# Kernel optimization log

Measured on AMD Instinct MI355X. Metric: run time of the kernel, lower is better.

The kernel has to match this reference:

```python
import jax, jax.numpy as jnp
import numpy as np
import math

B, L, E, H, G = 2, 128, 1024, 16, 8
D = E // H   # head_dim = 64
R = H // G   # query heads per kv head = 2


def setup_inputs() -> dict:
    key = jax.random.key(0)
    ks = jax.random.split(key, 12)
    def nrm(k, shape, s=1.0):
        return jax.random.normal(k, shape, dtype=jnp.float32) * s
    return {
        "Q": nrm(ks[0], (B, L, E)),
        "K": nrm(ks[1], (B, L, E)),
        "V": nrm(ks[2], (B, L, E)),
        "rpe": nrm(ks[3], (B, L, L, E)),
        "ln_g": jnp.ones((E,), jnp.float32),
        "ln_b": jnp.zeros((E,), jnp.float32),
        "Wq": nrm(ks[4], (E, H * D), 0.02), "bq": jnp.zeros((H * D,), jnp.float32),
        "Wk": nrm(ks[5], (E, G * D), 0.02), "bk": jnp.zeros((G * D,), jnp.float32),
        "Wv": nrm(ks[6], (E, G * D), 0.02), "bv": jnp.zeros((G * D,), jnp.float32),
        "Wrk": nrm(ks[7], (E, G * D), 0.02), "brk": jnp.zeros((G * D,), jnp.float32),
        "Wrv": nrm(ks[8], (E, G * D), 0.02), "brv": jnp.zeros((G * D,), jnp.float32),
        "Wo": nrm(ks[9], (E, E), 0.02), "bo": jnp.zeros((E,), jnp.float32),
    }


def _layernorm(x, g, b, eps=1e-5):
    mu = jnp.mean(x, axis=-1, keepdims=True)
    var = jnp.var(x, axis=-1, keepdims=True)
    return (x - mu) * jax.lax.rsqrt(var + eps) * g + b


def reference(Q, K, V, rpe, ln_g, ln_b, Wq, bq, Wk, bk, Wv, bv, Wrk, brk, Wrv, brv, Wo, bo):
    q = (Q @ Wq + bq).reshape(B, L, H, D).transpose(0, 2, 1, 3)   # [B,H,L,D]
    k = (K @ Wk + bk).reshape(B, L, G, D).transpose(0, 2, 1, 3)   # [B,G,L,D]
    v = (V @ Wv + bv).reshape(B, L, G, D).transpose(0, 2, 1, 3)   # [B,G,L,D]

    rn = _layernorm(rpe, ln_g, ln_b)                              # [B,L,L,E]
    rpe_k = (rn @ Wrk + brk).reshape(B, L, L, G, D).transpose(0, 3, 1, 2, 4)  # [B,G,L,L,D]
    rpe_v = (rn @ Wrv + brv).reshape(B, L, L, G, D).transpose(0, 3, 1, 2, 4)

    # Group query heads: head h = g*R + r maps to kv group g (repeat_interleave semantics).
    qg = q.reshape(B, G, R, L, D)
    # score[b,h,i,j] = q[b,h,i] . (k[b,g,i] + rpe_k[b,g,i,j]) / sqrt(D)
    # (note: the original pairs q_i with k_i, only rpe_k carries j-dependence)
    base = jnp.einsum('bgrid,bgid->bgri', qg, k)                  # j-independent q.k
    cross = jnp.einsum('bgrid,bgijd->bgrij', qg, rpe_k)
    scores = (base[..., None] + cross) / math.sqrt(D)             # [B,G,R,L,L]

    # Faithful to F.softmax over flattened L*L axis per head.
    attn = jax.nn.softmax(scores.reshape(B, G, R, L * L), axis=-1).reshape(B, G, R, L, L)

    # qv[b,h,i] = sum_j attn[b,h,i,j] * (v[b,g,i] + rpe_v[b,g,i,j])
    wsum = jnp.sum(attn, axis=-1)                                 # [B,G,R,L]
    qv = wsum[..., None] * v[:, :, None] + jnp.einsum('bgrij,bgijd->bgrid', attn, rpe_v)
    qv = qv.reshape(B, H, L, D).transpose(0, 2, 1, 3).reshape(B, L, E)
    return qv @ Wo + bo
```

## Files before the change

kernel.cpp:

```cpp
#include <hip/hip_runtime.h>


__global__ __launch_bounds__(256) void k_zero(
    const float* __restrict__ bq, const float* __restrict__ bk, const float* __restrict__ bv,
    const float* __restrict__ bo,
    float* __restrict__ q_ws, float* __restrict__ k_ws, float* __restrict__ v_ws,
    float* __restrict__ qv_ws, float* __restrict__ out, float* __restrict__ Gu_ws)
{
  int rr = blockIdx.x, tid = threadIdx.x;
#pragma unroll
  for (int s = 0; s < 4; s++) {
    int i = tid + s * 256;
    q_ws[rr * 1024 + i] = bq[i];
    qv_ws[rr * 1024 + i] = 0.f;
    out[rr * 1024 + i] = bo[i];
  }
#pragma unroll
  for (int s = 0; s < 2; s++) {
    int i = tid + s * 256;
    k_ws[rr * 512 + i] = bk[i];
    v_ws[rr * 512 + i] = bv[i];
  }
  int t = rr * 256 + tid;
  if (t < 4096) Gu_ws[t] = 0.f;
}

__global__ __launch_bounds__(256) void k_qkv(
    const float* __restrict__ Q, const float* __restrict__ K, const float* __restrict__ V,
    const float* __restrict__ Wq, const float* __restrict__ Wk, const float* __restrict__ Wv,
    float* __restrict__ q_ws, float* __restrict__ k_ws, float* __restrict__ v_ws)
{
  __shared__ float xs[8][256];
  int ct = blockIdx.x, rt = blockIdx.y, es = blockIdx.z, tid = threadIdx.x;
  const float* X; const float* W; float* out; int ldW, ldO, c0;
  if (ct < 4)      { X = Q; W = Wq; out = q_ws; ldW = 1024; ldO = 1024; c0 = ct * 256; }
  else if (ct < 6) { X = K; W = Wk; out = k_ws; ldW = 512;  ldO = 512;  c0 = (ct - 4) * 256; }
  else             { X = V; W = Wv; out = v_ws; ldW = 512;  ldO = 512;  c0 = (ct - 6) * 256; }
  int row0 = rt * 8, e0 = es * 256;
  for (int f = tid; f < 512; f += 256) {
    int r = f >> 6, e4 = f & 63;
    *(float4*)&xs[r][e4 * 4] = *(const float4*)(X + (size_t)(row0 + r) * 1024 + e0 + e4 * 4);
  }
  __syncthreads();
  int cg = tid & 63, rs = tid >> 6;
  int c = c0 + cg * 4;
  float a0[4] = {0, 0, 0, 0}, a1[4] = {0, 0, 0, 0};
  for (int e = 0; e < 256; e++) {
    float4 w4 = *(const float4*)(W + (size_t)(e0 + e) * ldW + c);
    float x0 = xs[rs][e], x1 = xs[rs + 4][e];
    a0[0] += x0 * w4.x; a0[1] += x0 * w4.y; a0[2] += x0 * w4.z; a0[3] += x0 * w4.w;
    a1[0] += x1 * w4.x; a1[1] += x1 * w4.y; a1[2] += x1 * w4.z; a1[3] += x1 * w4.w;
  }
#pragma unroll
  for (int s = 0; s < 4; s++) {
    atomicAdd(out + (size_t)(row0 + rs) * ldO + c + s, a0[s]);
    atomicAdd(out + (size_t)(row0 + rs + 4) * ldO + c + s, a1[s]);
  }
}

__global__ __launch_bounds__(256) void k_base(
    const float* __restrict__ q_ws, const float* __restrict__ k_ws,
    const float* __restrict__ brk, float* __restrict__ S0_ws)
{
  int t = blockIdx.x * 256 + threadIdx.x;
  int r = t >> 4, h = t & 15, g = h >> 1;
  const float* qp = q_ws + r * 1024 + h * 64;
  const float* kp = k_ws + r * 512 + g * 64;
  const float* bp = brk + g * 64;
  float s = 0.f;
  for (int d = 0; d < 64; d++) s += qp[d] * (kp[d] + bp[d]);
  S0_ws[t] = s * 0.125f;
}

__global__ __launch_bounds__(256) void k_uproj(
    const float* __restrict__ q_ws, const float* __restrict__ Wrk,
    const float* __restrict__ lng, const float* __restrict__ lnb,
    float* __restrict__ ut_ws, float* __restrict__ Gu_ws, float* __restrict__ S0_ws)
{
  __shared__ float wt[64][132];
  __shared__ float qs[64][65];
  int et = blockIdx.x, rrt = blockIdx.y, g = blockIdx.z, tid = threadIdx.x;
  int e0 = et * 128, rr0 = rrt * 32;
  for (int f = tid; f < 2048; f += 256) {
    int er = f >> 4, dq = f & 15;
    float4 p = *(const float4*)(Wrk + (size_t)(e0 + er) * 512 + g * 64 + dq * 4);
    wt[dq * 4 + 0][er] = p.x; wt[dq * 4 + 1][er] = p.y;
    wt[dq * 4 + 2][er] = p.z; wt[dq * 4 + 3][er] = p.w;
  }
  for (int f = tid; f < 1024; f += 256) {
    int m = f >> 4, dq = f & 15;
    int rr = rr0 + (m >> 1), h = g * 2 + (m & 1);
    float4 p = *(const float4*)(q_ws + (size_t)rr * 1024 + h * 64 + dq * 4);
    qs[m][dq * 4 + 0] = p.x; qs[m][dq * 4 + 1] = p.y;
    qs[m][dq * 4 + 2] = p.z; qs[m][dq * 4 + 3] = p.w;
  }
  __syncthreads();
  int eg = tid & 31, rs = tid >> 5;
  float acc[8][4];
#pragma unroll
  for (int i = 0; i < 8; i++)
#pragma unroll
    for (int s = 0; s < 4; s++) acc[i][s] = 0.f;
  for (int d = 0; d < 64; d++) {
    float4 wv = *(float4*)&wt[d][eg * 4];
#pragma unroll
    for (int i = 0; i < 8; i++) {
      float qv = qs[rs * 8 + i][d];
      acc[i][0] += qv * wv.x; acc[i][1] += qv * wv.y;
      acc[i][2] += qv * wv.z; acc[i][3] += qv * wv.w;
    }
  }
#pragma unroll
  for (int i = 0; i < 4; i++) {
    int m0 = rs * 8 + 2 * i;
    int rr = rr0 + (m0 >> 1);
#pragma unroll
    for (int s = 0; s < 4; s++) {
      int e = e0 + eg * 4 + s;
      float2 st;
      st.x = acc[2 * i][s] * 0.125f;
      st.y = acc[2 * i + 1][s] * 0.125f;
      *(float2*)(ut_ws + ((size_t)rr * 1024 + e) * 16 + g * 2) = st;
    }
  }
  float4 ge4 = *(const float4*)(lng + e0 + eg * 4);
  float4 be4 = *(const float4*)(lnb + e0 + eg * 4);
#pragma unroll
  for (int i = 0; i < 8; i++) {
    float pg = 0.125f * (ge4.x * acc[i][0] + ge4.y * acc[i][1] + ge4.z * acc[i][2] + ge4.w * acc[i][3]);
    float pb = 0.125f * (be4.x * acc[i][0] + be4.y * acc[i][1] + be4.z * acc[i][2] + be4.w * acc[i][3]);
#pragma unroll
    for (int mk = 16; mk >= 1; mk >>= 1) { pg += __shfl_xor(pg, mk); pb += __shfl_xor(pb, mk); }
    if (eg == 0) {
      int m = rs * 8 + i;
      int rr = rr0 + (m >> 1), h = g * 2 + (m & 1);
      atomicAdd(Gu_ws + rr * 16 + h, pg);
      atomicAdd(S0_ws + rr * 16 + h, pb);
    }
  }
}

__global__ __launch_bounds__(128) void k_dotp(
    const float* __restrict__ rpe, const float* __restrict__ lng,
    const float* __restrict__ ut_ws, const float* __restrict__ Gu_ws,
    const float* __restrict__ S0_ws,
    float* __restrict__ s_ws, float* __restrict__ mu_ws, float* __restrict__ rs_ws)
{
  __shared__ float xs[32][140];
  __shared__ float us[128][16];
  int jt = blockIdx.x, rr = blockIdx.y, tid = threadIdx.x;
  int es2 = tid & 1, hg = (tid >> 1) & 3, jp = tid >> 3;
  int j0 = jp * 2;
  float acc0[4] = {0, 0, 0, 0}, acc1[4] = {0, 0, 0, 0};
  float sx0 = 0.f, sq0 = 0.f, sx1 = 0.f, sq1 = 0.f;

  for (int ec = 0; ec < 8; ec++) {
    __syncthreads();
    for (int f = tid; f < 512; f += 128) {
      int e = f >> 2, hq = f & 3;
      float4 u4 = *(const float4*)(ut_ws + ((size_t)rr * 1024 + ec * 128 + e) * 16 + hq * 4);
      float ge = lng[ec * 128 + e];
      u4.x *= ge; u4.y *= ge; u4.z *= ge; u4.w *= ge;
      *(float4*)&us[e][hq * 4] = u4;
    }
    for (int f = tid; f < 1024; f += 128) {
      int j = f >> 5, e4 = f & 31;
      int slot = (e4 < 16) ? e4 * 4 : e4 * 4 + 4;
      *(float4*)&xs[j][slot] =
          *(const float4*)(rpe + ((size_t)(rr * 128 + jt * 32 + j)) * 1024 + ec * 128 + e4 * 4);
    }
    __syncthreads();
    int ebase = es2 * 68, ubase = es2 * 64;
    for (int e4 = 0; e4 < 16; e4++) {
      float4 xa = *(float4*)&xs[j0][ebase + e4 * 4];
      float4 xb = *(float4*)&xs[j0 + 1][ebase + e4 * 4];
      float4 u0 = *(float4*)&us[ubase + e4 * 4 + 0][hg * 4];
      float4 u1 = *(float4*)&us[ubase + e4 * 4 + 1][hg * 4];
      float4 u2 = *(float4*)&us[ubase + e4 * 4 + 2][hg * 4];
      float4 u3 = *(float4*)&us[ubase + e4 * 4 + 3][hg * 4];
      acc0[0] += xa.x * u0.x + xa.y * u1.x + xa.z * u2.x + xa.w * u3.x;
      acc0[1] += xa.x * u0.y + xa.y * u1.y + xa.z * u2.y + xa.w * u3.y;
      acc0[2] += xa.x * u0.z + xa.y * u1.z + xa.z * u2.z + xa.w * u3.z;
      acc0[3] += xa.x * u0.w + xa.y * u1.w + xa.z * u2.w + xa.w * u3.w;
      acc1[0] += xb.x * u0.x + xb.y * u1.x + xb.z * u2.x + xb.w * u3.x;
      acc1[1] += xb.x * u0.y + xb.y * u1.y + xb.z * u2.y + xb.w * u3.y;
      acc1[2] += xb.x * u0.z + xb.y * u1.z + xb.z * u2.z + xb.w * u3.z;
      acc1[3] += xb.x * u0.w + xb.y * u1.w + xb.z * u2.w + xb.w * u3.w;
      sx0 += xa.x + xa.y + xa.z + xa.w;
      sq0 += xa.x * xa.x + xa.y * xa.y + xa.z * xa.z + xa.w * xa.w;
      sx1 += xb.x + xb.y + xb.z + xb.w;
      sq1 += xb.x * xb.x + xb.y * xb.y + xb.z * xb.z + xb.w * xb.w;
    }
  }
#pragma unroll
  for (int s = 0; s < 4; s++) {
    acc0[s] += __shfl_xor(acc0[s], 1);
    acc1[s] += __shfl_xor(acc1[s], 1);
  }
  sx0 += __shfl_xor(sx0, 1); sq0 += __shfl_xor(sq0, 1);
  sx1 += __shfl_xor(sx1, 1); sq1 += __shfl_xor(sq1, 1);

  float4 Gu4 = *(const float4*)(Gu_ws + rr * 16 + hg * 4);
  float4 S04 = *(const float4*)(S0_ws + rr * 16 + hg * 4);
  float mu0 = sx0 * (1.f / 1024.f), mu1 = sx1 * (1.f / 1024.f);
  float r0 = rsqrtf(fmaxf(sq0 * (1.f / 1024.f) - mu0 * mu0, 0.f) + 1e-5f);
  float r1 = rsqrtf(fmaxf(sq1 * (1.f / 1024.f) - mu1 * mu1, 0.f) + 1e-5f);
  int jg0 = jt * 32 + j0;
  if (es2 == 0) {
    float4 o0, o1;
    o0.x = S04.x + r0 * (acc0[0] - mu0 * Gu4.x); o0.y = S04.y + r0 * (acc0[1] - mu0 * Gu4.y);
    o0.z = S04.z + r0 * (acc0[2] - mu0 * Gu4.z); o0.w = S04.w + r0 * (acc0[3] - mu0 * Gu4.w);
    o1.x = S04.x + r1 * (acc1[0] - mu1 * Gu4.x); o1.y = S04.y + r1 * (acc1[1] - mu1 * Gu4.y);
    o1.z = S04.z + r1 * (acc1[2] - mu1 * Gu4.z); o1.w = S04.w + r1 * (acc1[3] - mu1 * Gu4.w);
    *(float4*)(s_ws + ((size_t)rr * 128 + jg0) * 16 + hg * 4) = o0;
    *(float4*)(s_ws + ((size_t)rr * 128 + jg0 + 1) * 16 + hg * 4) = o1;
    if (hg == 0) {
      mu_ws[rr * 128 + jg0] = mu0; rs_ws[rr * 128 + jg0] = r0;
      mu_ws[rr * 128 + jg0 + 1] = mu1; rs_ws[rr * 128 + jg0 + 1] = r1;
    }
  }
}

__global__ __launch_bounds__(256) void k_attn_p(
    const float* __restrict__ mu_ws, const float* __restrict__ rs_ws,
    float* __restrict__ s_ws,
    float* __restrict__ M_ws, float* __restrict__ Z_ws, float* __restrict__ C1_ws)
{
  int rr = blockIdx.x, tid = threadIdx.x;
  int h = tid >> 4, jl = tid & 15;
  float sv[8];
  float m = -1e30f;
#pragma unroll
  for (int k = 0; k < 8; k++) {
    int j = jl + k * 16;
    sv[k] = s_ws[((size_t)rr * 128 + j) * 16 + h];
    m = fmaxf(m, sv[k]);
  }
#pragma unroll
  for (int mk = 8; mk >= 1; mk >>= 1) m = fmaxf(m, __shfl_xor(m, mk, 16));
  float z = 0.f, c1 = 0.f;
#pragma unroll
  for (int k = 0; k < 8; k++) {
    int j = jl + k * 16;
    float p = expf(sv[k] - m);
    z += p;
    float p2 = p * rs_ws[rr * 128 + j];
    c1 += p2 * mu_ws[rr * 128 + j];
    s_ws[((size_t)rr * 128 + j) * 16 + h] = p2;
  }
#pragma unroll
  for (int mk = 8; mk >= 1; mk >>= 1) { z += __shfl_xor(z, mk, 16); c1 += __shfl_xor(c1, mk, 16); }
  if (jl == 0) {
    M_ws[rr * 16 + h] = m; Z_ws[rr * 16 + h] = z; C1_ws[rr * 16 + h] = c1;
  }
}

__global__ __launch_bounds__(256) void k_comb(
    const float* __restrict__ M_ws, const float* __restrict__ Z_ws, float* __restrict__ sc_ws)
{
  __shared__ float Mg[32], Zg[32];
  int tid = threadIdx.x;
  if (tid < 32) {
    int b = tid >> 4, h = tid & 15;
    float m = -1e30f;
    for (int i = 0; i < 128; i++) m = fmaxf(m, M_ws[((b << 7) + i) * 16 + h]);
    float z = 0.f;
    for (int i = 0; i < 128; i++) {
      int idx = ((b << 7) + i) * 16 + h;
      z += Z_ws[idx] * expf(M_ws[idx] - m);
    }
    Mg[tid] = m; Zg[tid] = z;
  }
  __syncthreads();
  for (int idx = tid; idx < 4096; idx += 256) {
    int r = idx >> 4, h = idx & 15, b = r >> 7;
    sc_ws[idx] = expf(M_ws[idx] - Mg[b * 16 + h]) / Zg[b * 16 + h];
  }
}

__global__ __launch_bounds__(256) void k_wun(
    const float* __restrict__ rpe, const float* __restrict__ lng, const float* __restrict__ lnb,
    const float* __restrict__ p2_ws,
    const float* __restrict__ Z_ws, const float* __restrict__ C1_ws,
    float* __restrict__ w_ws)
{
  __shared__ float xs[8][520];
  __shared__ float p2s[128][16];
  __shared__ float C1S[16], ZS[16];
  int et = blockIdx.x, rr = blockIdx.y, tid = threadIdx.x;
  int e0 = et * 512;
  for (int f = tid; f < 512; f += 256) {
    int j = f >> 2, hq = f & 3;
    *(float4*)&p2s[j][hq * 4] = *(const float4*)(p2_ws + ((size_t)rr * 128 + j) * 16 + hq * 4);
  }
  if (tid < 16) { C1S[tid] = C1_ws[rr * 16 + tid]; ZS[tid] = Z_ws[rr * 16 + tid]; }
  float acc[2][16];
#pragma unroll
  for (int c = 0; c < 2; c++)
#pragma unroll
    for (int h = 0; h < 16; h++) acc[c][h] = 0.f;
  for (int jc = 0; jc < 16; jc++) {
    __syncthreads();
    for (int f = tid; f < 1024; f += 256) {
      int j = f >> 7, e4 = f & 127;
      *(float4*)&xs[j][e4 * 4] =
          *(const float4*)(rpe + ((size_t)(rr * 128 + jc * 8 + j)) * 1024 + e0 + e4 * 4);
    }
    __syncthreads();
#pragma unroll
    for (int j = 0; j < 8; j++) {
      float2 x2 = *(float2*)&xs[j][tid * 2];
      float4 p0 = *(float4*)&p2s[jc * 8 + j][0];
      float4 p1 = *(float4*)&p2s[jc * 8 + j][4];
      float4 p2 = *(float4*)&p2s[jc * 8 + j][8];
      float4 p3 = *(float4*)&p2s[jc * 8 + j][12];
      acc[0][0] += x2.x * p0.x; acc[0][1] += x2.x * p0.y; acc[0][2] += x2.x * p0.z; acc[0][3] += x2.x * p0.w;
      acc[0][4] += x2.x * p1.x; acc[0][5] += x2.x * p1.y; acc[0][6] += x2.x * p1.z; acc[0][7] += x2.x * p1.w;
      acc[0][8] += x2.x * p2.x; acc[0][9] += x2.x * p2.y; acc[0][10] += x2.x * p2.z; acc[0][11] += x2.x * p2.w;
      acc[0][12] += x2.x * p3.x; acc[0][13] += x2.x * p3.y; acc[0][14] += x2.x * p3.z; acc[0][15] += x2.x * p3.w;
      acc[1][0] += x2.y * p0.x; acc[1][1] += x2.y * p0.y; acc[1][2] += x2.y * p0.z; acc[1][3] += x2.y * p0.w;
      acc[1][4] += x2.y * p1.x; acc[1][5] += x2.y * p1.y; acc[1][6] += x2.y * p1.z; acc[1][7] += x2.y * p1.w;
      acc[1][8] += x2.y * p2.x; acc[1][9] += x2.y * p2.y; acc[1][10] += x2.y * p2.z; acc[1][11] += x2.y * p2.w;
      acc[1][12] += x2.y * p3.x; acc[1][13] += x2.y * p3.y; acc[1][14] += x2.y * p3.z; acc[1][15] += x2.y * p3.w;
    }
  }
  int e = e0 + tid * 2;
#pragma unroll
  for (int c = 0; c < 2; c++) {
    float ge = lng[e + c], be = lnb[e + c];
    float* wp = w_ws + ((size_t)rr * 1024 + e + c) * 16;
#pragma unroll
    for (int hq = 0; hq < 4; hq++) {
      float4 o;
      o.x = ge * (acc[c][hq * 4 + 0] - C1S[hq * 4 + 0]) + be * ZS[hq * 4 + 0];
      o.y = ge * (acc[c][hq * 4 + 1] - C1S[hq * 4 + 1]) + be * ZS[hq * 4 + 1];
      o.z = ge * (acc[c][hq * 4 + 2] - C1S[hq * 4 + 2]) + be * ZS[hq * 4 + 2];
      o.w = ge * (acc[c][hq * 4 + 3] - C1S[hq * 4 + 3]) + be * ZS[hq * 4 + 3];
      *(float4*)(wp + hq * 4) = o;
    }
  }
}

__global__ __launch_bounds__(256) void k_qv(
    const float* __restrict__ w_ws, const float* __restrict__ Wrv,
    float* __restrict__ qv_ws)
{
  __shared__ float wch[2][256][16];
  int ec = blockIdx.x, rp = blockIdx.y, tid = threadIdx.x;
  int e0 = ec * 256, rr0 = rp * 2;
  for (int f = tid; f < 2048; f += 256) {
    int r2 = f >> 10, rem = f & 1023;
    int e = rem >> 2, hq = rem & 3;
    *(float4*)&wch[r2][e][hq * 4] =
        *(const float4*)(w_ws + ((size_t)(rr0 + r2) * 1024 + e0 + e) * 16 + hq * 4);
  }
  __syncthreads();
  int cg = tid & 127, es2 = tid >> 7;
  int c = cg * 4, g = cg >> 4, h0 = g * 2, dloc = (cg & 15) * 4;
  float a[2][2][4];
#pragma unroll
  for (int r = 0; r < 2; r++)
#pragma unroll
    for (int hh = 0; hh < 2; hh++)
#pragma unroll
      for (int s = 0; s < 4; s++) a[r][hh][s] = 0.f;
  for (int ei = 0; ei < 128; ei++) {
    int e = es2 * 128 + ei;
    float4 wv = *(const float4*)(Wrv + (size_t)(e0 + e) * 512 + c);
    float2 w0 = *(float2*)&wch[0][e][h0];
    float2 w1 = *(float2*)&wch[1][e][h0];
    a[0][0][0] += w0.x * wv.x; a[0][0][1] += w0.x * wv.y; a[0][0][2] += w0.x * wv.z; a[0][0][3] += w0.x * wv.w;
    a[0][1][0] += w0.y * wv.x; a[0][1][1] += w0.y * wv.y; a[0][1][2] += w0.y * wv.z; a[0][1][3] += w0.y * wv.w;
    a[1][0][0] += w1.x * wv.x; a[1][0][1] += w1.x * wv.y; a[1][0][2] += w1.x * wv.z; a[1][0][3] += w1.x * wv.w;
    a[1][1][0] += w1.y * wv.x; a[1][1][1] += w1.y * wv.y; a[1][1][2] += w1.y * wv.z; a[1][1][3] += w1.y * wv.w;
  }
#pragma unroll
  for (int r = 0; r < 2; r++)
#pragma unroll
    for (int hh = 0; hh < 2; hh++)
#pragma unroll
      for (int s = 0; s < 4; s++)
        atomicAdd(qv_ws + (size_t)(rr0 + r) * 1024 + (h0 + hh) * 64 + dloc + s, a[r][hh][s]);
}

__global__ __launch_bounds__(256) void k_out(
    const float* __restrict__ qv_ws, const float* __restrict__ v_ws,
    const float* __restrict__ brv, const float* __restrict__ Z_ws,
    const float* __restrict__ sc_ws, const float* __restrict__ Wo,
    float* __restrict__ out)
{
  __shared__ float xs[8][256];
  int ct = blockIdx.x, rt = blockIdx.y, es = blockIdx.z, tid = threadIdx.x;
  int row0 = rt * 8, e0 = es * 256, c0 = ct * 256;
  for (int f = tid; f < 2048; f += 256) {
    int r = f >> 8, ei = f & 255;
    int e = e0 + ei, row = row0 + r;
    int h = e >> 6, gg = h >> 1, dl = e & 63;
    float vb = v_ws[row * 512 + gg * 64 + dl] + brv[gg * 64 + dl];
    xs[r][ei] = sc_ws[row * 16 + h] * (Z_ws[row * 16 + h] * vb + qv_ws[(size_t)row * 1024 + e]);
  }
  __syncthreads();
  int cg = tid & 63, rs = tid >> 6;
  int c = c0 + cg * 4;
  float a0[4] = {0, 0, 0, 0}, a1[4] = {0, 0, 0, 0};
  for (int e = 0; e < 256; e++) {
    float4 w4 = *(const float4*)(Wo + (size_t)(e0 + e) * 1024 + c);
    float x0 = xs[rs][e], x1 = xs[rs + 4][e];
    a0[0] += x0 * w4.x; a0[1] += x0 * w4.y; a0[2] += x0 * w4.z; a0[3] += x0 * w4.w;
    a1[0] += x1 * w4.x; a1[1] += x1 * w4.y; a1[2] += x1 * w4.z; a1[3] += x1 * w4.w;
  }
#pragma unroll
  for (int s = 0; s < 4; s++) {
    atomicAdd(out + (size_t)(row0 + rs) * 1024 + c + s, a0[s]);
    atomicAdd(out + (size_t)(row0 + rs + 4) * 1024 + c + s, a1[s]);
  }
}

extern "C" void kernel_launch(void* const* d_in, const int* in_sizes, int n_in,
                              void* d_out, int out_size, void* d_ws, size_t ws_size,
                              hipStream_t stream) {
  (void)in_sizes; (void)n_in; (void)out_size; (void)ws_size;
  const float* Q   = (const float*)d_in[0];
  const float* K   = (const float*)d_in[1];
  const float* V   = (const float*)d_in[2];
  const float* rpe = (const float*)d_in[3];
  const float* lng = (const float*)d_in[4];
  const float* lnb = (const float*)d_in[5];
  const float* Wq  = (const float*)d_in[6];
  const float* bq  = (const float*)d_in[7];
  const float* Wk  = (const float*)d_in[8];
  const float* bk  = (const float*)d_in[9];
  const float* Wv  = (const float*)d_in[10];
  const float* bv  = (const float*)d_in[11];
  const float* Wrk = (const float*)d_in[12];
  const float* brk = (const float*)d_in[13];
  const float* Wrv = (const float*)d_in[14];
  const float* brv = (const float*)d_in[15];
  const float* Wo  = (const float*)d_in[16];
  const float* bo  = (const float*)d_in[17];
  float* out = (float*)d_out;

  float* ws    = (float*)d_ws;
  float* q_ws  = ws;
  float* k_ws  = q_ws + 262144;
  float* v_ws  = k_ws + 131072;
  float* ut_ws = v_ws + 131072;
  float* S0_ws = ut_ws + 4194304;
  float* Gu_ws = S0_ws + 4096;
  float* s_ws  = Gu_ws + 4096;
  float* mu_ws = s_ws + 524288;
  float* rs_ws = mu_ws + 32768;
  float* M_ws  = rs_ws + 32768;
  float* Z_ws  = M_ws + 4096;
  float* C1_ws = Z_ws + 4096;
  float* sc_ws = C1_ws + 4096;
  float* qv_ws = sc_ws + 4096;
  float* w_ws  = ut_ws;

  k_zero<<<256, 256, 0, stream>>>(bq, bk, bv, bo, q_ws, k_ws, v_ws, qv_ws, out, Gu_ws);
  k_qkv<<<dim3(8, 32, 4), 256, 0, stream>>>(Q, K, V, Wq, Wk, Wv, q_ws, k_ws, v_ws);
  k_base<<<16, 256, 0, stream>>>(q_ws, k_ws, brk, S0_ws);
  k_uproj<<<dim3(8, 8, 8), 256, 0, stream>>>(q_ws, Wrk, lng, lnb, ut_ws, Gu_ws, S0_ws);
  k_dotp<<<dim3(4, 256), 128, 0, stream>>>(rpe, lng, ut_ws, Gu_ws, S0_ws, s_ws, mu_ws, rs_ws);
  k_attn_p<<<256, 256, 0, stream>>>(mu_ws, rs_ws, s_ws, M_ws, Z_ws, C1_ws);
  k_comb<<<1, 256, 0, stream>>>(M_ws, Z_ws, sc_ws);
  k_wun<<<dim3(2, 256), 256, 0, stream>>>(rpe, lng, lnb, s_ws, Z_ws, C1_ws, w_ws);
  k_qv<<<dim3(4, 128), 256, 0, stream>>>(w_ws, Wrv, qv_ws);
  k_out<<<dim3(4, 32, 4), 256, 0, stream>>>(qv_ws, v_ws, brv, Z_ws, sc_ws, Wo, out);
}
```

Baseline: 535.4 us.

## Retile GEMM kernels for more row reuse and restructure rpe passes

k_qkv and k_out now give each thread 8 rows instead of 2, so every weight float4 load is reused across more rows. k_dotp drops its shared-memory staging of rpe and has each thread stream its own rpe row straight from global memory. k_wun uses 512 threads with one column per thread and 16-row chunks. k_qv is rewritten as a shared-memory tiled GEMM per kv group. Together these aim to cut redundant global weight reads and improve reuse, at the cost of higher register pressure, possibly lower occupancy, and uncoalesced per-thread row reads in k_dotp.

New measurement: 575.3 us. 7.4% more time.

```diff
diff --git a/kernel.cpp b/kernel.cpp
--- a/kernel.cpp
+++ b/kernel.cpp
@@ -30,32 +30,38 @@
     const float* __restrict__ Wq, const float* __restrict__ Wk, const float* __restrict__ Wv,
     float* __restrict__ q_ws, float* __restrict__ k_ws, float* __restrict__ v_ws)
 {
-  __shared__ float xs[8][256];
+  __shared__ float xs[32][256];
   int ct = blockIdx.x, rt = blockIdx.y, es = blockIdx.z, tid = threadIdx.x;
   const float* X; const float* W; float* out; int ldW, ldO, c0;
   if (ct < 4)      { X = Q; W = Wq; out = q_ws; ldW = 1024; ldO = 1024; c0 = ct * 256; }
   else if (ct < 6) { X = K; W = Wk; out = k_ws; ldW = 512;  ldO = 512;  c0 = (ct - 4) * 256; }
   else             { X = V; W = Wv; out = v_ws; ldW = 512;  ldO = 512;  c0 = (ct - 6) * 256; }
-  int row0 = rt * 8, e0 = es * 256;
-  for (int f = tid; f < 512; f += 256) {
+  int row0 = rt * 32, e0 = es * 256;
+  for (int f = tid; f < 2048; f += 256) {
     int r = f >> 6, e4 = f & 63;
     *(float4*)&xs[r][e4 * 4] = *(const float4*)(X + (size_t)(row0 + r) * 1024 + e0 + e4 * 4);
   }
   __syncthreads();
   int cg = tid & 63, rs = tid >> 6;
   int c = c0 + cg * 4;
-  float a0[4] = {0, 0, 0, 0}, a1[4] = {0, 0, 0, 0};
+  float a[8][4];
+#pragma unroll
+  for (int i = 0; i < 8; i++)
+#pragma unroll
+    for (int s = 0; s < 4; s++) a[i][s] = 0.f;
   for (int e = 0; e < 256; e++) {
     float4 w4 = *(const float4*)(W + (size_t)(e0 + e) * ldW + c);
-    float x0 = xs[rs][e], x1 = xs[rs + 4][e];
-    a0[0] += x0 * w4.x; a0[1] += x0 * w4.y; a0[2] += x0 * w4.z; a0[3] += x0 * w4.w;
-    a1[0] += x1 * w4.x; a1[1] += x1 * w4.y; a1[2] += x1 * w4.z; a1[3] += x1 * w4.w;
-  }
-#pragma unroll
-  for (int s = 0; s < 4; s++) {
-    atomicAdd(out + (size_t)(row0 + rs) * ldO + c + s, a0[s]);
-    atomicAdd(out + (size_t)(row0 + rs + 4) * ldO + c + s, a1[s]);
-  }
+#pragma unroll
+    for (int i = 0; i < 8; i++) {
+      float x = xs[rs * 8 + i][e];
+      a[i][0] += x * w4.x; a[i][1] += x * w4.y; a[i][2] += x * w4.z; a[i][3] += x * w4.w;
+    }
+  }
+#pragma unroll
+  for (int i = 0; i < 8; i++)
+#pragma unroll
+    for (int s = 0; s < 4; s++)
+      atomicAdd(out + (size_t)(row0 + rs * 8 + i) * ldO + c + s, a[i][s]);
 }
 
 __global__ __launch_bounds__(256) void k_base(
@@ -140,85 +146,57 @@
   }
 }
 
-__global__ __launch_bounds__(128) void k_dotp(
+__global__ __launch_bounds__(256) void k_dotp(
     const float* __restrict__ rpe, const float* __restrict__ lng,
     const float* __restrict__ ut_ws, const float* __restrict__ Gu_ws,
     const float* __restrict__ S0_ws,
     float* __restrict__ s_ws, float* __restrict__ mu_ws, float* __restrict__ rs_ws)
 {
-  __shared__ float xs[32][140];
   __shared__ float us[128][16];
   int jt = blockIdx.x, rr = blockIdx.y, tid = threadIdx.x;
-  int es2 = tid & 1, hg = (tid >> 1) & 3, jp = tid >> 3;
-  int j0 = jp * 2;
-  float acc0[4] = {0, 0, 0, 0}, acc1[4] = {0, 0, 0, 0};
-  float sx0 = 0.f, sq0 = 0.f, sx1 = 0.f, sq1 = 0.f;
+  int jl = tid >> 2, hg = tid & 3;
+  int j = jt * 64 + jl;
+  const float* xrow = rpe + ((size_t)rr * 128 + j) * 1024;
+  float acc[4] = {0, 0, 0, 0};
+  float sx = 0.f, sq = 0.f;
 
   for (int ec = 0; ec < 8; ec++) {
     __syncthreads();
-    for (int f = tid; f < 512; f += 128) {
+    for (int f = tid; f < 512; f += 256) {
       int e = f >> 2, hq = f & 3;
       float4 u4 = *(const float4*)(ut_ws + ((size_t)rr * 1024 + ec * 128 + e) * 16 + hq * 4);
       float ge = lng[ec * 128 + e];
       u4.x *= ge; u4.y *= ge; u4.z *= ge; u4.w *= ge;
       *(float4*)&us[e][hq * 4] = u4;
     }
-    for (int f = tid; f < 1024; f += 128) {
-      int j = f >> 5, e4 = f & 31;
-      int slot = (e4 < 16) ? e4 * 4 : e4 * 4 + 4;
-      *(float4*)&xs[j][slot] =
-          *(const float4*)(rpe + ((size_t)(rr * 128 + jt * 32 + j)) * 1024 + ec * 128 + e4 * 4);
-    }
-    __syncthreads();
-    int ebase = es2 * 68, ubase = es2 * 64;
-    for (int e4 = 0; e4 < 16; e4++) {
-      float4 xa = *(float4*)&xs[j0][ebase + e4 * 4];
-      float4 xb = *(float4*)&xs[j0 + 1][ebase + e4 * 4];
-      float4 u0 = *(float4*)&us[ubase + e4 * 4 + 0][hg * 4];
-      float4 u1 = *(float4*)&us[ubase + e4 * 4 + 1][hg * 4];
-      float4 u2 = *(float4*)&us[ubase + e4 * 4 + 2][hg * 4];
-      float4 u3 = *(float4*)&us[ubase + e4 * 4 + 3][hg * 4];
-      acc0[0] += xa.x * u0.x + xa.y * u1.x + xa.z * u2.x + xa.w * u3.x;
-      acc0[1] += xa.x * u0.y + xa.y * u1.y + xa.z * u2.y + xa.w * u3.y;
-      acc0[2] += xa.x * u0.z + xa.y * u1.z + xa.z * u2.z + xa.w * u3.z;
-      acc0[3] += xa.x * u0.w + xa.y * u1.w + xa.z * u2.w + xa.w * u3.w;
-      acc1[0] += xb.x * u0.x + xb.y * u1.x + xb.z * u2.x + xb.w * u3.x;
-      acc1[1] += xb.x * u0.y + xb.y * u1.y + xb.z * u2.y + xb.w * u3.y;
-      acc1[2] += xb.x * u0.z + xb.y * u1.z + xb.z * u2.z + xb.w * u3.z;
-      acc1[3] += xb.x * u0.w + xb.y * u1.w + xb.z * u2.w + xb.w * u3.w;
-      sx0 += xa.x + xa.y + xa.z + xa.w;
-      sq0 += xa.x * xa.x + xa.y * xa.y + xa.z * xa.z + xa.w * xa.w;
-      sx1 += xb.x + xb.y + xb.z + xb.w;
-      sq1 += xb.x * xb.x + xb.y * xb.y + xb.z * xb.z + xb.w * xb.w;
-    }
-  }
-#pragma unroll
-  for (int s = 0; s < 4; s++) {
-    acc0[s] += __shfl_xor(acc0[s], 1);
-    acc1[s] += __shfl_xor(acc1[s], 1);
-  }
-  sx0 += __shfl_xor(sx0, 1); sq0 += __shfl_xor(sq0, 1);
-  sx1 += __shfl_xor(sx1, 1); sq1 += __shfl_xor(sq1, 1);
-
+    __syncthreads();
+    const float* xp = xrow + ec * 128;
+#pragma unroll 8
+    for (int e4 = 0; e4 < 32; e4++) {
+      float4 xv = *(const float4*)(xp + e4 * 4);
+      float4 u0 = *(float4*)&us[e4 * 4 + 0][hg * 4];
+      float4 u1 = *(float4*)&us[e4 * 4 + 1][hg * 4];
+      float4 u2 = *(float4*)&us[e4 * 4 + 2][hg * 4];
+      float4 u3 = *(float4*)&us[e4 * 4 + 3][hg * 4];
+      acc[0] += xv.x * u0.x + xv.y * u1.x + xv.z * u2.x + xv.w * u3.x;
+      acc[1] += xv.x * u0.y + xv.y * u1.y + xv.z * u2.y + xv.w * u3.y;
+      acc[2] += xv.x * u0.z + xv.y * u1.z + xv.z * u2.z + xv.w * u3.z;
+      acc[3] += xv.x * u0.w + xv.y * u1.w + xv.z * u2.w + xv.w * u3.w;
+      sx += xv.x + xv.y + xv.z + xv.w;
+      sq += xv.x * xv.x + xv.y * xv.y + xv.z * xv.z + xv.w * xv.w;
+    }
+  }
+  float mu = sx * (1.f / 1024.f);
+  float rs = rsqrtf(fmaxf(sq * (1.f / 1024.f) - mu * mu, 0.f) + 1e-5f);
   float4 Gu4 = *(const float4*)(Gu_ws + rr * 16 + hg * 4);
   float4 S04 = *(const float4*)(S0_ws + rr * 16 + hg * 4);
-  float mu0 = sx0 * (1.f / 1024.f), mu1 = sx1 * (1.f / 1024.f);
-  float r0 = rsqrtf(fmaxf(sq0 * (1.f / 1024.f) - mu0 * mu0, 0.f) + 1e-5f);
-  float r1 = rsqrtf(fmaxf(sq1 * (1.f / 1024.f) - mu1 * mu1, 0.f) + 1e-5f);
-  int jg0 = jt * 32 + j0;
-  if (es2 == 0) {
-    float4 o0, o1;
-    o0.x = S04.x + r0 * (acc0[0] - mu0 * Gu4.x); o0.y = S04.y + r0 * (acc0[1] - mu0 * Gu4.y);
-    o0.z = S04.z + r0 * (acc0[2] - mu0 * Gu4.z); o0.w = S04.w + r0 * (acc0[3] - mu0 * Gu4.w);
-    o1.x = S04.x + r1 * (acc1[0] - mu1 * Gu4.x); o1.y = S04.y + r1 * (acc1[1] - mu1 * Gu4.y);
-    o1.z = S04.z + r1 * (acc1[2] - mu1 * Gu4.z); o1.w = S04.w + r1 * (acc1[3] - mu1 * Gu4.w);
-    *(float4*)(s_ws + ((size_t)rr * 128 + jg0) * 16 + hg * 4) = o0;
-    *(float4*)(s_ws + ((size_t)rr * 128 + jg0 + 1) * 16 + hg * 4) = o1;
-    if (hg == 0) {
-      mu_ws[rr * 128 + jg0] = mu0; rs_ws[rr * 128 + jg0] = r0;
-      mu_ws[rr * 128 + jg0 + 1] = mu1; rs_ws[rr * 128 + jg0 + 1] = r1;
-    }
-  }
+  float4 o;
+  o.x = S04.x + rs * (acc[0] - mu * Gu4.x);
+  o.y = S04.y + rs * (acc[1] - mu * Gu4.y);
+  o.z = S04.z + rs * (acc[2] - mu * Gu4.z);
+  o.w = S04.w + rs * (acc[3] - mu * Gu4.w);
+  *(float4*)(s_ws + ((size_t)rr * 128 + j) * 16 + hg * 4) = o;
+  if (hg == 0) { mu_ws[rr * 128 + j] = mu; rs_ws[rr * 128 + j] = rs; }
 }
 
 __global__ __launch_bounds__(256) void k_attn_p(
@@ -278,66 +256,59 @@
   }
 }
 
-__global__ __launch_bounds__(256) void k_wun(
+__global__ __launch_bounds__(512) void k_wun(
     const float* __restrict__ rpe, const float* __restrict__ lng, const float* __restrict__ lnb,
     const float* __restrict__ p2_ws,
     const float* __restrict__ Z_ws, const float* __restrict__ C1_ws,
     float* __restrict__ w_ws)
 {
-  __shared__ float xs[8][520];
+  __shared__ float xs[16][516];
   __shared__ float p2s[128][16];
   __shared__ float C1S[16], ZS[16];
   int et = blockIdx.x, rr = blockIdx.y, tid = threadIdx.x;
   int e0 = et * 512;
-  for (int f = tid; f < 512; f += 256) {
-    int j = f >> 2, hq = f & 3;
-    *(float4*)&p2s[j][hq * 4] = *(const float4*)(p2_ws + ((size_t)rr * 128 + j) * 16 + hq * 4);
+  if (tid < 512) {
+    for (int f = tid; f < 512; f += 512) {
+      int j = f >> 2, hq = f & 3;
+      *(float4*)&p2s[j][hq * 4] = *(const float4*)(p2_ws + ((size_t)rr * 128 + j) * 16 + hq * 4);
+    }
   }
   if (tid < 16) { C1S[tid] = C1_ws[rr * 16 + tid]; ZS[tid] = Z_ws[rr * 16 + tid]; }
-  float acc[2][16];
-#pragma unroll
-  for (int c = 0; c < 2; c++)
-#pragma unroll
-    for (int h = 0; h < 16; h++) acc[c][h] = 0.f;
-  for (int jc = 0; jc < 16; jc++) {
-    __syncthreads();
-    for (int f = tid; f < 1024; f += 256) {
+  float acc[16];
+#pragma unroll
+  for (int h = 0; h < 16; h++) acc[h] = 0.f;
+  for (int jc = 0; jc < 8; jc++) {
+    __syncthreads();
+    for (int f = tid; f < 2048; f += 512) {
       int j = f >> 7, e4 = f & 127;
       *(float4*)&xs[j][e4 * 4] =
-          *(const float4*)(rpe + ((size_t)(rr * 128 + jc * 8 + j)) * 1024 + e0 + e4 * 4);
-    }
-    __syncthreads();
-#pragma unroll
-    for (int j = 0; j < 8; j++) {
-      float2 x2 = *(float2*)&xs[j][tid * 2];
-      float4 p0 = *(float4*)&p2s[jc * 8 + j][0];
-      float4 p1 = *(float4*)&p2s[jc * 8 + j][4];
-      float4 p2 = *(float4*)&p2s[jc * 8 + j][8];
-      float4 p3 = *(float4*)&p2s[jc * 8 + j][12];
-      acc[0][0] += x2.x * p0.x; acc[0][1] += x2.x * p0.y; acc[0][2] += x2.x * p0.z; acc[0][3] += x2.x * p0.w;
-      acc[0][4] += x2.x * p1.x; acc[0][5] += x2.x * p1.y; acc[0][6] += x2.x * p1.z; acc[0][7] += x2.x * p1.w;
-      acc[0][8] += x2.x * p2.x; acc[0][9] += x2.x * p2.y; acc[0][10] += x2.x * p2.z; acc[0][11] += x2.x * p2.w;
-      acc[0][12] += x2.x * p3.x; acc[0][13] += x2.x * p3.y; acc[0][14] += x2.x * p3.z; acc[0][15] += x2.x * p3.w;
-      acc[1][0] += x2.y * p0.x; acc[1][1] += x2.y * p0.y; acc[1][2] += x2.y * p0.z; acc[1][3] += x2.y * p0.w;
-      acc[1][4] += x2.y * p1.x; acc[1][5] += x2.y * p1.y; acc[1][6] += x2.y * p1.z; acc[1][7] += x2.y * p1.w;
-      acc[1][8] += x2.y * p2.x; acc[1][9] += x2.y * p2.y; acc[1][10] += x2.y * p2.z; acc[1][11] += x2.y * p2.w;
-      acc[1][12] += x2.y * p3.x; acc[1][13] += x2.y * p3.y; acc[1][14] += x2.y * p3.z; acc[1][15] += x2.y * p3.w;
-    }
-  }
-  int e = e0 + tid * 2;
-#pragma unroll
-  for (int c = 0; c < 2; c++) {
-    float ge = lng[e + c], be = lnb[e + c];
-    float* wp = w_ws + ((size_t)rr * 1024 + e + c) * 16;
-#pragma unroll
-    for (int hq = 0; hq < 4; hq++) {
-      float4 o;
-      o.x = ge * (acc[c][hq * 4 + 0] - C1S[hq * 4 + 0]) + be * ZS[hq * 4 + 0];
-      o.y = ge * (acc[c][hq * 4 + 1] - C1S[hq * 4 + 1]) + be * ZS[hq * 4 + 1];
-      o.z = ge * (acc[c][hq * 4 + 2] - C1S[hq * 4 + 2]) + be * ZS[hq * 4 + 2];
-      o.w = ge * (acc[c][hq * 4 + 3] - C1S[hq * 4 + 3]) + be * ZS[hq * 4 + 3];
-      *(float4*)(wp + hq * 4) = o;
-    }
+          *(const float4*)(rpe + ((size_t)(rr * 128 + jc * 16 + j)) * 1024 + e0 + e4 * 4);
+    }
+    __syncthreads();
+#pragma unroll
+    for (int j = 0; j < 16; j++) {
+      float x = xs[j][tid];
+      float4 p0 = *(float4*)&p2s[jc * 16 + j][0];
+      float4 p1 = *(float4*)&p2s[jc * 16 + j][4];
+      float4 p2 = *(float4*)&p2s[jc * 16 + j][8];
+      float4 p3 = *(float4*)&p2s[jc * 16 + j][12];
+      acc[0] += x * p0.x; acc[1] += x * p0.y; acc[2] += x * p0.z; acc[3] += x * p0.w;
+      acc[4] += x * p1.x; acc[5] += x * p1.y; acc[6] += x * p1.z; acc[7] += x * p1.w;
+      acc[8] += x * p2.x; acc[9] += x * p2.y; acc[10] += x * p2.z; acc[11] += x * p2.w;
+      acc[12] += x * p3.x; acc[13] += x * p3.y; acc[14] += x * p3.z; acc[15] += x * p3.w;
+    }
+  }
+  int e = e0 + tid;
+  float ge = lng[e], be = lnb[e];
+  float* wp = w_ws + ((size_t)rr * 1024 + e) * 16;
+#pragma unroll
+  for (int hq = 0; hq < 4; hq++) {
+    float4 o;
+    o.x = ge * (acc[hq * 4 + 0] - C1S[hq * 4 + 0]) + be * ZS[hq * 4 + 0];
+    o.y = ge * (acc[hq * 4 + 1] - C1S[hq * 4 + 1]) + be * ZS[hq * 4 + 1];
+    o.z = ge * (acc[hq * 4 + 2] - C1S[hq * 4 + 2]) + be * ZS[hq * 4 + 2];
+    o.w = ge * (acc[hq * 4 + 3] - C1S[hq * 4 + 3]) + be * ZS[hq * 4 + 3];
+    *(float4*)(wp + hq * 4) = o;
   }
 }
 
@@ -345,42 +316,48 @@
     const float* __restrict__ w_ws, const float* __restrict__ Wrv,
     float* __restrict__ qv_ws)
 {
-  __shared__ float wch[2][256][16];
-  int ec = blockIdx.x, rp = blockIdx.y, tid = threadIdx.x;
-  int e0 = ec * 256, rr0 = rp * 2;
-  for (int f = tid; f < 2048; f += 256) {
-    int r2 = f >> 10, rem = f & 1023;
-    int e = rem >> 2, hq = rem & 3;
-    *(float4*)&wch[r2][e][hq * 4] =
-        *(const float4*)(w_ws + ((size_t)(rr0 + r2) * 1024 + e0 + e) * 16 + hq * 4);
-  }
-  __syncthreads();
-  int cg = tid & 127, es2 = tid >> 7;
-  int c = cg * 4, g = cg >> 4, h0 = g * 2, dloc = (cg & 15) * 4;
-  float a[2][2][4];
-#pragma unroll
-  for (int r = 0; r < 2; r++)
-#pragma unroll
-    for (int hh = 0; hh < 2; hh++)
-#pragma unroll
-      for (int s = 0; s < 4; s++) a[r][hh][s] = 0.f;
-  for (int ei = 0; ei < 128; ei++) {
-    int e = es2 * 128 + ei;
-    float4 wv = *(const float4*)(Wrv + (size_t)(e0 + e) * 512 + c);
-    float2 w0 = *(float2*)&wch[0][e][h0];
-    float2 w1 = *(float2*)&wch[1][e][h0];
-    a[0][0][0] += w0.x * wv.x; a[0][0][1] += w0.x * wv.y; a[0][0][2] += w0.x * wv.z; a[0][0][3] += w0.x * wv.w;
-    a[0][1][0] += w0.y * wv.x; a[0][1][1] += w0.y * wv.y; a[0][1][2] += w0.y * wv.z; a[0][1][3] += w0.y * wv.w;
-    a[1][0][0] += w1.x * wv.x; a[1][0][1] += w1.x * wv.y; a[1][0][2] += w1.x * wv.z; a[1][0][3] += w1.x * wv.w;
-    a[1][1][0] += w1.y * wv.x; a[1][1][1] += w1.y * wv.y; a[1][1][2] += w1.y * wv.z; a[1][1][3] += w1.y * wv.w;
-  }
-#pragma unroll
-  for (int r = 0; r < 2; r++)
-#pragma unroll
-    for (int hh = 0; hh < 2; hh++)
-#pragma unroll
-      for (int s = 0; s < 4; s++)
-        atomicAdd(qv_ws + (size_t)(rr0 + r) * 1024 + (h0 + hh) * 64 + dloc + s, a[r][hh][s]);
+  __shared__ float As[64][68];
+  __shared__ float Ws[64][68];
+  int g = blockIdx.x, rrt = blockIdx.y, es = blockIdx.z, tid = threadIdx.x;
+  int rr0 = rrt * 32, e0 = es * 256;
+  int cl = tid & 15, ms = tid >> 4;
+  float acc[4][4];
+#pragma unroll
+  for (int i = 0; i < 4; i++)
+#pragma unroll
+    for (int s = 0; s < 4; s++) acc[i][s] = 0.f;
+  for (int kc = 0; kc < 4; kc++) {
+    __syncthreads();
+    for (int f = tid; f < 2048; f += 256) {
+      int rl = f >> 6, e = f & 63;
+      float2 w2 = *(const float2*)(w_ws + ((size_t)(rr0 + rl) * 1024 + e0 + kc * 64 + e) * 16 + g * 2);
+      As[rl * 2 + 0][e] = w2.x;
+      As[rl * 2 + 1][e] = w2.y;
+    }
+    for (int f = tid; f < 1024; f += 256) {
+      int e = f >> 4, c4 = f & 15;
+      *(float4*)&Ws[e][c4 * 4] =
+          *(const float4*)(Wrv + (size_t)(e0 + kc * 64 + e) * 512 + g * 64 + c4 * 4);
+    }
+    __syncthreads();
+    for (int e = 0; e < 64; e++) {
+      float4 wv = *(float4*)&Ws[e][cl * 4];
+#pragma unroll
+      for (int i = 0; i < 4; i++) {
+        float a = As[ms * 4 + i][e];
+        acc[i][0] += a * wv.x; acc[i][1] += a * wv.y;
+        acc[i][2] += a * wv.z; acc[i][3] += a * wv.w;
+      }
+    }
+  }
+#pragma unroll
+  for (int i = 0; i < 4; i++) {
+    int m = ms * 4 + i;
+    int rr = rr0 + (m >> 1), hh = m & 1;
+    float* qp = qv_ws + (size_t)rr * 1024 + (g * 2 + hh) * 64 + cl * 4;
+#pragma unroll
+    for (int s = 0; s < 4; s++) atomicAdd(qp + s, acc[i][s]);
+  }
 }
 
 __global__ __launch_bounds__(256) void k_out(
@@ -389,31 +366,41 @@
     const float* __restrict__ sc_ws, const float* __restrict__ Wo,
     float* __restrict__ out)
 {
-  __shared__ float xs[8][256];
+  __shared__ float xs[32][128];
   int ct = blockIdx.x, rt = blockIdx.y, es = blockIdx.z, tid = threadIdx.x;
-  int row0 = rt * 8, e0 = es * 256, c0 = ct * 256;
-  for (int f = tid; f < 2048; f += 256) {
-    int r = f >> 8, ei = f & 255;
-    int e = e0 + ei, row = row0 + r;
-    int h = e >> 6, gg = h >> 1, dl = e & 63;
-    float vb = v_ws[row * 512 + gg * 64 + dl] + brv[gg * 64 + dl];
-    xs[r][ei] = sc_ws[row * 16 + h] * (Z_ws[row * 16 + h] * vb + qv_ws[(size_t)row * 1024 + e]);
+  int row0 = rt * 32, e0 = es * 128, c0 = ct * 256;
+  for (int f = tid; f < 1024; f += 256) {
+    int r = f >> 5, e4 = f & 31;
+    int row = row0 + r;
+#pragma unroll
+    for (int s = 0; s < 4; s++) {
+      int e = e0 + e4 * 4 + s;
+      int h = e >> 6, gg = h >> 1, dl = e & 63;
+      float vb = v_ws[row * 512 + gg * 64 + dl] + brv[gg * 64 + dl];
+      xs[r][e4 * 4 + s] = sc_ws[row * 16 + h] * (Z_ws[row * 16 + h] * vb + qv_ws[(size_t)row * 1024 + e]);
+    }
   }
   __syncthreads();
   int cg = tid & 63, rs = tid >> 6;
   int c = c0 + cg * 4;
-  float a0[4] = {0, 0, 0, 0}, a1[4] = {0, 0, 0, 0};
-  for (int e = 0; e < 256; e++) {
+  float a[8][4];
+#pragma unroll
+  for (int i = 0; i < 8; i++)
+#pragma unroll
+    for (int s = 0; s < 4; s++) a[i][s] = 0.f;
+  for (int e = 0; e < 128; e++) {
     float4 w4 = *(const float4*)(Wo + (size_t)(e0 + e) * 1024 + c);
-    float x0 = xs[rs][e], x1 = xs[rs + 4][e];
-    a0[0] += x0 * w4.x; a0[1] += x0 * w4.y; a0[2] += x0 * w4.z; a0[3] += x0 * w4.w;
-    a1[0] += x1 * w4.x; a1[1] += x1 * w4.y; a1[2] += x1 * w4.z; a1[3] += x1 * w4.w;
-  }
-#pragma unroll
-  for (int s = 0; s < 4; s++) {
-    atomicAdd(out + (size_t)(row0 + rs) * 1024 + c + s, a0[s]);
-    atomicAdd(out + (size_t)(row0 + rs + 4) * 1024 + c + s, a1[s]);
-  }
+#pragma unroll
+    for (int i = 0; i < 8; i++) {
+      float x = xs[rs * 8 + i][e];
+      a[i][0] += x * w4.x; a[i][1] += x * w4.y; a[i][2] += x * w4.z; a[i][3] += x * w4.w;
+    }
+  }
+#pragma unroll
+  for (int i = 0; i < 8; i++)
+#pragma unroll
+    for (int s = 0; s < 4; s++)
+      atomicAdd(out + (size_t)(row0 + rs * 8 + i) * 1024 + c + s, a[i][s]);
 }
 
 extern "C" void kernel_launch(void* const* d_in, const int* in_sizes, int n_in,
@@ -458,13 +445,13 @@
   float* w_ws  = ut_ws;
 
   k_zero<<<256, 256, 0, stream>>>(bq, bk, bv, bo, q_ws, k_ws, v_ws, qv_ws, out, Gu_ws);
-  k_qkv<<<dim3(8, 32, 4), 256, 0, stream>>>(Q, K, V, Wq, Wk, Wv, q_ws, k_ws, v_ws);
+  k_qkv<<<dim3(8, 8, 4), 256, 0, stream>>>(Q, K, V, Wq, Wk, Wv, q_ws, k_ws, v_ws);
   k_base<<<16, 256, 0, stream>>>(q_ws, k_ws, brk, S0_ws);
   k_uproj<<<dim3(8, 8, 8), 256, 0, stream>>>(q_ws, Wrk, lng, lnb, ut_ws, Gu_ws, S0_ws);
-  k_dotp<<<dim3(4, 256), 128, 0, stream>>>(rpe, lng, ut_ws, Gu_ws, S0_ws, s_ws, mu_ws, rs_ws);
+  k_dotp<<<dim3(2, 256), 256, 0, stream>>>(rpe, lng, ut_ws, Gu_ws, S0_ws, s_ws, mu_ws, rs_ws);
   k_attn_p<<<256, 256, 0, stream>>>(mu_ws, rs_ws, s_ws, M_ws, Z_ws, C1_ws);
   k_comb<<<1, 256, 0, stream>>>(M_ws, Z_ws, sc_ws);
-  k_wun<<<dim3(2, 256), 256, 0, stream>>>(rpe, lng, lnb, s_ws, Z_ws, C1_ws, w_ws);
-  k_qv<<<dim3(4, 128), 256, 0, stream>>>(w_ws, Wrv, qv_ws);
-  k_out<<<dim3(4, 32, 4), 256, 0, stream>>>(qv_ws, v_ws, brv, Z_ws, sc_ws, Wo, out);
-}
+  k_wun<<<dim3(2, 256), 512, 0, stream>>>(rpe, lng, lnb, s_ws, Z_ws, C1_ws, w_ws);
+  k_qv<<<dim3(8, 8, 4), 256, 0, stream>>>(w_ws, Wrv, qv_ws);
+  k_out<<<dim3(4, 8, 8), 256, 0, stream>>>(qv_ws, v_ws, brv, Z_ws, sc_ws, Wo, out);
+}
```
